# Optimization experiments

Hardware: AMD Instinct MI355X
Metric: run time of the kernel (lower is better)

The kernel has to match this reference:

```python
import jax, jax.numpy as jnp
import numpy as np

NUM_GRAPHS = 500
BN_EPS = 1e-5


def setup_inputs() -> dict:
    key = jax.random.key(0)
    ks = jax.random.split(key, 16)
    N, E, F, D, L = 100000, 1600000, 128, 128, 3
    x = jax.random.normal(ks[0], (N, F), dtype=jnp.float32)
    edge_index = jax.random.randint(ks[1], (2, E), 0, N)
    batch = jnp.sort(jax.random.randint(ks[2], (N,), 0, NUM_GRAPHS))
    s = 1.0 / np.sqrt(F)
    sd = 1.0 / np.sqrt(D)
    # SAGEConv layer 0: out = lin_l(mean_aggr(x_j)) + lin_r(x)
    sage_Wl = jax.random.uniform(ks[3], (F, D), jnp.float32, -s, s)
    sage_bl = jax.random.uniform(ks[4], (D,), jnp.float32, -s, s)
    sage_Wr = jax.random.uniform(ks[5], (F, D), jnp.float32, -s, s)
    # GINConv layers 1..L-1: nn = Linear(D,D) -> ReLU -> Linear(D,D)
    gin_W1 = jax.random.uniform(ks[6], (L - 1, D, D), jnp.float32, -sd, sd)
    gin_b1 = jax.random.uniform(ks[7], (L - 1, D), jnp.float32, -sd, sd)
    gin_W2 = jax.random.uniform(ks[8], (L - 1, D, D), jnp.float32, -sd, sd)
    gin_b2 = jax.random.uniform(ks[9], (L - 1, D), jnp.float32, -sd, sd)
    bn_gamma = jnp.ones((L, D), dtype=jnp.float32)
    bn_beta = jnp.zeros((L, D), dtype=jnp.float32)
    return {"x": x, "edge_index": edge_index, "batch": batch,
            "sage_Wl": sage_Wl, "sage_bl": sage_bl, "sage_Wr": sage_Wr,
            "gin_W1": gin_W1, "gin_b1": gin_b1, "gin_W2": gin_W2, "gin_b2": gin_b2,
            "bn_gamma": bn_gamma, "bn_beta": bn_beta}


def _batchnorm(h, gamma, beta):
    mu = jnp.mean(h, axis=0)
    var = jnp.var(h, axis=0)  # biased, as torch BN uses for normalization
    return (h - mu) * jax.lax.rsqrt(var + BN_EPS) * gamma + beta


def reference(x, edge_index, batch, sage_Wl, sage_bl, sage_Wr,
              gin_W1, gin_b1, gin_W2, gin_b2, bn_gamma, bn_beta):
    N = x.shape[0]
    src, dst = edge_index[0], edge_index[1]
    L = bn_gamma.shape[0]

    # Layer 0: SAGEConv (mean aggregation, root weight, no bias on lin_r)
    deg = jax.ops.segment_sum(jnp.ones_like(dst, dtype=x.dtype), dst, num_segments=N)
    aggr = jax.ops.segment_sum(x[src], dst, num_segments=N)
    aggr = aggr / jnp.maximum(deg, 1.0)[:, None]
    h = aggr @ sage_Wl + sage_bl + x @ sage_Wr
    h = jax.nn.relu(h)
    h = _batchnorm(h, bn_gamma[0], bn_beta[0])
    xs = [h]

    # Layers 1..L-1: GINConv (eps=0): nn(x + sum_aggr(x_j))
    for i in range(1, L):
        aggr = jax.ops.segment_sum(h[src], dst, num_segments=N)
        t = h + aggr
        t = jax.nn.relu(t @ gin_W1[i - 1] + gin_b1[i - 1])
        t = t @ gin_W2[i - 1] + gin_b2[i - 1]
        h = jax.nn.relu(t)
        h = _batchnorm(h, bn_gamma[i], bn_beta[i])
        xs.append(h)

    # pooling != 'last': concat global_add_pool over every layer
    pooled = jnp.concatenate(
        [jax.ops.segment_sum(xi, batch, num_segments=NUM_GRAPHS) for xi in xs], axis=1)
    node_feats = jnp.concatenate(xs, axis=1)
    return (pooled, node_feats)
```

## Files before the change

kernel.cpp:

```cpp
#include <hip/hip_runtime.h>
#include <hip/hip_bf16.h>


#define BN_EPS 1e-5f
#define EPB 4096

typedef short s8v __attribute__((ext_vector_type(8)));
typedef float f4v __attribute__((ext_vector_type(4)));

__device__ __forceinline__ float bflo(unsigned u) { return __uint_as_float(u << 16); }
__device__ __forceinline__ float bfhi(unsigned u) { return __uint_as_float(u & 0xffff0000u); }
__device__ __forceinline__ unsigned short f2bf(float f) {
    unsigned u = __float_as_uint(f);
    unsigned r = (u + 0x7fffu + ((u >> 16) & 1u)) >> 16;
    return (unsigned short)r;
}
__device__ __forceinline__ unsigned pk2(float a, float b) {
    return (unsigned)f2bf(a) | ((unsigned)f2bf(b) << 16);
}
__device__ __forceinline__ void unpack8(uint4 u, float* v) {
    v[0] = bflo(u.x); v[1] = bfhi(u.x);
    v[2] = bflo(u.y); v[3] = bfhi(u.y);
    v[4] = bflo(u.z); v[5] = bfhi(u.z);
    v[6] = bflo(u.w); v[7] = bfhi(u.w);
}


__global__ __launch_bounds__(256) void k_binA(const int* __restrict__ src,
                                              const int* __restrict__ dst, int E, int NB, int CAP,
                                              int* __restrict__ bcnt,
                                              unsigned long long* __restrict__ ebuf) {
    __shared__ int hist[512], base[512], cur[512];
    const int tid = threadIdx.x;
    const int e0 = blockIdx.x * EPB;
    for (int i = tid; i < 512; i += 256) { hist[i] = 0; cur[i] = 0; }
    __syncthreads();
#pragma unroll
    for (int k = 0; k < EPB / 256; k++) {
        int e = e0 + k * 256 + tid;
        if (e < E) atomicAdd(&hist[dst[e] >> 8], 1);
    }
    __syncthreads();
    for (int b = tid; b < NB; b += 256)
        base[b] = hist[b] ? atomicAdd(&bcnt[b], hist[b]) : 0;
    __syncthreads();
#pragma unroll
    for (int k = 0; k < EPB / 256; k++) {
        int e = e0 + k * 256 + tid;
        if (e < E) {
            int d = dst[e];
            int b = d >> 8;
            int lp = atomicAdd(&cur[b], 1);
            int gp = base[b] + lp;
            if (gp < CAP)
                ebuf[(size_t)b * CAP + gp] = ((unsigned long long)d << 32) | (unsigned)src[e];
        }
    }
}

__global__ __launch_bounds__(256) void k_binB(const unsigned long long* __restrict__ ebuf,
                                              int CAP, const int* __restrict__ bcnt,
                                              int N, int E,
                                              int* __restrict__ rp, int* __restrict__ csr) {
    __shared__ int deg[256], sc[256], cur[256];
    __shared__ int s_cbase;
    const int tid = threadIdx.x;
    const int b = blockIdx.x;
    const int cnt = min(bcnt[b], CAP);

    int partial = 0;
    for (int i = tid; i < b; i += 256) partial += bcnt[i];
    sc[tid] = partial;
    __syncthreads();
    for (int off = 128; off > 0; off >>= 1) {
        if (tid < off) sc[tid] += sc[tid + off];
        __syncthreads();
    }
    if (tid == 0) s_cbase = sc[0];
    __syncthreads();
    const int cbase = s_cbase;

    deg[tid] = 0;
    __syncthreads();
    const unsigned long long* eb = ebuf + (size_t)b * CAP;
    for (int i = tid; i < cnt; i += 256) {
        int d = (int)(eb[i] >> 32);
        atomicAdd(&deg[d & 255], 1);
    }
    __syncthreads();
    int myDeg = deg[tid];
    sc[tid] = myDeg;
    __syncthreads();
    for (int off = 1; off < 256; off <<= 1) {
        int v = (tid >= off) ? sc[tid - off] : 0;
        __syncthreads();
        sc[tid] += v;
        __syncthreads();
    }
    int pos = cbase + sc[tid] - myDeg;
    int node = b * 256 + tid;
    if (node < N) rp[node] = pos;
    cur[tid] = pos;
    __syncthreads();
    for (int i = tid; i < cnt; i += 256) {
        unsigned long long e = eb[i];
        int d = (int)(e >> 32);
        int p = atomicAdd(&cur[d & 255], 1);
        csr[p] = (int)(e & 0xffffffffu);
    }
    if (b == 0 && tid == 0) rp[N] = E;
}


__global__ __launch_bounds__(256) void k_prep(
    const float* __restrict__ sWl, const float* __restrict__ sWr,
    const float* __restrict__ gW1, const float* __restrict__ gW2,
    unsigned short* __restrict__ Wp,
    const float* __restrict__ x, uint4* __restrict__ tb, int n16,
    uint4* __restrict__ pool4, int npool4, int zpb,
    uint4* __restrict__ zreg4, int nzreg4) {
    const int b = blockIdx.x;
    const int tid = threadIdx.x;
    if (b < 384) {
        int wsel = b >> 6;
        int idx = (b & 63) * 256 + tid;
        const float* W;
        switch (wsel) {
            case 0: W = sWl; break;
            case 1: W = sWr; break;
            case 2: W = gW1; break;
            case 3: W = gW2; break;
            case 4: W = gW1 + 16384; break;
            default: W = gW2 + 16384; break;
        }
        int k = idx >> 7, d = idx & 127;
        float w = W[idx];
        unsigned short h = f2bf(w);
        float hf = __uint_as_float((unsigned)h << 16);
        unsigned short l = f2bf(w - hf);
        int o = (((k >> 3) * 128) + d) * 8 + (k & 7);
        unsigned short* slot = Wp + (size_t)wsel * 32768;
        slot[o] = h;
        slot[16384 + o] = l;
    } else if (b < 384 + zpb) {
        int i = (b - 384) * 256 + tid;
        if (i < npool4) pool4[i] = make_uint4(0, 0, 0, 0);
    } else if (b == 384 + zpb) {
        for (int i = tid; i < nzreg4; i += 256) zreg4[i] = make_uint4(0, 0, 0, 0);
    } else {
        int i = (b - 385 - zpb) * 256 + tid;
        if (i >= n16) return;
        const float4* p = reinterpret_cast<const float4*>(x) + (size_t)i * 2;
        float4 a = p[0], bb = p[1];
        uint4 o;
        o.x = pk2(a.x, a.y); o.y = pk2(a.z, a.w);
        o.z = pk2(bb.x, bb.y); o.w = pk2(bb.z, bb.w);
        tb[i] = o;
    }
}


template <bool SELF, bool MEAN>
__global__ __launch_bounds__(256) void k_aggr(const int* __restrict__ rp,
                                              const int* __restrict__ csr,
                                              const uint4* __restrict__ src,
                                              uint4* __restrict__ out, int N) {
    const int node = blockIdx.x * 4 + (threadIdx.x >> 6);
    if (node >= N) return;
    const int lane = threadIdx.x & 63;
    const int c = lane & 15, grp = lane >> 4;

    float acc[8];
#pragma unroll
    for (int k = 0; k < 8; k++) acc[k] = 0.f;

    const int lo = rp[node], hi = rp[node + 1];
    int j = lo + grp;
    for (; j + 12 < hi; j += 16) {
        int sn0 = csr[j];
        int sn1 = csr[j + 4];
        int sn2 = csr[j + 8];
        int sn3 = csr[j + 12];
        uint4 r0 = src[(size_t)sn0 * 16 + c];
        uint4 r1 = src[(size_t)sn1 * 16 + c];
        uint4 r2 = src[(size_t)sn2 * 16 + c];
        uint4 r3 = src[(size_t)sn3 * 16 + c];
        float v[8];
        unpack8(r0, v);
#pragma unroll
        for (int k = 0; k < 8; k++) acc[k] += v[k];
        unpack8(r1, v);
#pragma unroll
        for (int k = 0; k < 8; k++) acc[k] += v[k];
        unpack8(r2, v);
#pragma unroll
        for (int k = 0; k < 8; k++) acc[k] += v[k];
        unpack8(r3, v);
#pragma unroll
        for (int k = 0; k < 8; k++) acc[k] += v[k];
    }
    for (; j + 4 < hi; j += 8) {
        int sn0 = csr[j];
        int sn1 = csr[j + 4];
        uint4 r0 = src[(size_t)sn0 * 16 + c];
        uint4 r1 = src[(size_t)sn1 * 16 + c];
        float v[8];
        unpack8(r0, v);
#pragma unroll
        for (int k = 0; k < 8; k++) acc[k] += v[k];
        unpack8(r1, v);
#pragma unroll
        for (int k = 0; k < 8; k++) acc[k] += v[k];
    }
    if (j < hi) {
        float v[8];
        unpack8(src[(size_t)csr[j] * 16 + c], v);
#pragma unroll
        for (int k = 0; k < 8; k++) acc[k] += v[k];
    }

#pragma unroll
    for (int k = 0; k < 8; k++) {
        acc[k] += __shfl_xor(acc[k], 16, 64);
        acc[k] += __shfl_xor(acc[k], 32, 64);
    }

    if (grp == 0) {
        if (SELF) {
            float v[8];
            unpack8(src[(size_t)node * 16 + c], v);
#pragma unroll
            for (int k = 0; k < 8; k++) acc[k] += v[k];
        }
        if (MEAN) {
            float inv = 1.0f / fmaxf((float)(hi - lo), 1.0f);
#pragma unroll
            for (int k = 0; k < 8; k++) acc[k] *= inv;
        }
        uint4 o;
        o.x = pk2(acc[0], acc[1]); o.y = pk2(acc[2], acc[3]);
        o.z = pk2(acc[4], acc[5]); o.w = pk2(acc[6], acc[7]);
        out[(size_t)node * 16 + c] = o;
    }
}


#define MFMA_STAGE(Whi, Wlo, B0, B1, ACC)                                          \
    _Pragma("unroll")                                                              \
    for (int ks = 0; ks < 4; ks++) {                                               \
        s8v b0 = __builtin_bit_cast(s8v, B0[ks]);                                  \
        s8v b1 = __builtin_bit_cast(s8v, B1[ks]);                                  \
        _Pragma("unroll")                                                          \
        for (int df = 0; df < 8; df++) {                                           \
            int wi = (ks * 4 + lg) * 128 + df * 16 + l16;                          \
            s8v ah = __builtin_bit_cast(s8v, Whi[wi]);                             \
            s8v al = __builtin_bit_cast(s8v, Wlo[wi]);                             \
            ACC[0][df] = __builtin_amdgcn_mfma_f32_16x16x32_bf16(ah, b0, ACC[0][df], 0, 0, 0); \
            ACC[1][df] = __builtin_amdgcn_mfma_f32_16x16x32_bf16(ah, b1, ACC[1][df], 0, 0, 0); \
            ACC[0][df] = __builtin_amdgcn_mfma_f32_16x16x32_bf16(al, b0, ACC[0][df], 0, 0, 0); \
            ACC[1][df] = __builtin_amdgcn_mfma_f32_16x16x32_bf16(al, b1, ACC[1][df], 0, 0, 0); \
        }                                                                          \
    }

#define STATS_EPILOGUE(OO, V0, V1)                                                 \
    {                                                                              \
        _Pragma("unroll")                                                          \
        for (int df = 0; df < 8; df++) {                                           \
            float s[4], q[4];                                                      \
            _Pragma("unroll")                                                      \
            for (int r = 0; r < 4; r++) {                                          \
                float a0 = V0 ? (&OO[0][df].x)[r] : 0.f;                           \
                float a1 = V1 ? (&OO[1][df].x)[r] : 0.f;                           \
                s[r] = a0 + a1;                                                    \
                q[r] = a0 * a0 + a1 * a1;                                          \
            }                                                                      \
            _Pragma("unroll")                                                      \
            for (int m = 1; m < 16; m <<= 1) {                                     \
                _Pragma("unroll")                                                  \
                for (int r = 0; r < 4; r++) {                                      \
                    s[r] += __shfl_xor(s[r], m, 64);                               \
                    q[r] += __shfl_xor(q[r], m, 64);                               \
                }                                                                  \
            }                                                                      \
            if (l16 == 0) {                                                        \
                _Pragma("unroll")                                                  \
                for (int r = 0; r < 4; r++) {                                      \
                    sred[wid][df * 16 + lg * 4 + r][0] = s[r];                     \
                    sred[wid][df * 16 + lg * 4 + r][1] = q[r];                     \
                }                                                                  \
            }                                                                      \
        }                                                                          \
        __syncthreads();                                                           \
        if (tid < 128) {                                                           \
            float s = sred[0][tid][0] + sred[1][tid][0] + sred[2][tid][0] + sred[3][tid][0]; \
            float q = sred[0][tid][1] + sred[1][tid][1] + sred[2][tid][1] + sred[3][tid][1]; \
            unsafeAtomicAdd(&gsum[tid], s);                                        \
            unsafeAtomicAdd(&gsq[tid], q);                                         \
        }                                                                          \
    }


__global__ __launch_bounds__(256) void k_gemm_sage(
    const uint4* __restrict__ A1, const uint4* __restrict__ A2,
    const uint4* __restrict__ Wfrag,
    const float* __restrict__ bias,
    float* __restrict__ outF, float* __restrict__ gsum, float* __restrict__ gsq,
    int N) {
    __shared__ float sred[4][128][2];
    const int tid = threadIdx.x;
    const int lane = tid & 63, wid = tid >> 6;
    const int nbase = blockIdx.x * 128 + wid * 32;
    const int l16 = lane & 15, lg = lane >> 4;

    f4v acc[2][8];
#pragma unroll
    for (int nf = 0; nf < 2; nf++)
#pragma unroll
        for (int df = 0; df < 8; df++)
            acc[nf][df] = (f4v){0.f, 0.f, 0.f, 0.f};

#pragma unroll
    for (int t = 0; t < 2; t++) {
        const uint4* A = t ? A2 : A1;
        const uint4* Whi = Wfrag + (size_t)t * 4096;
        const uint4* Wlo = Whi + 2048;
        uint4 bvec[2][4];
#pragma unroll
        for (int nf = 0; nf < 2; nf++) {
            const uint4* row = A + (size_t)(nbase + nf * 16 + l16) * 16;
#pragma unroll
            for (int ks = 0; ks < 4; ks++) bvec[nf][ks] = row[ks * 4 + lg];
        }
        MFMA_STAGE(Whi, Wlo, bvec[0], bvec[1], acc)
    }

    const bool v0 = (nbase + l16) < N;
    const bool v1 = (nbase + 16 + l16) < N;
    float4 oo[2][8];
#pragma unroll
    for (int df = 0; df < 8; df++) {
        int d0 = df * 16 + lg * 4;
        const float4 bb = *reinterpret_cast<const float4*>(bias + d0);
#pragma unroll
        for (int nf = 0; nf < 2; nf++) {
            oo[nf][df].x = fmaxf(acc[nf][df][0] + bb.x, 0.f);
            oo[nf][df].y = fmaxf(acc[nf][df][1] + bb.y, 0.f);
            oo[nf][df].z = fmaxf(acc[nf][df][2] + bb.z, 0.f);
            oo[nf][df].w = fmaxf(acc[nf][df][3] + bb.w, 0.f);
        }
    }

    STATS_EPILOGUE(oo, v0, v1)

#pragma unroll
    for (int nf = 0; nf < 2; nf++) {
        int n = nbase + nf * 16 + l16;
        if (n < N) {
#pragma unroll
            for (int df = 0; df < 8; df++)
                *reinterpret_cast<float4*>(outF + (size_t)n * 384 + df * 16 + lg * 4) = oo[nf][df];
        }
    }
}


__global__ __launch_bounds__(256) void k_gemm_gin(
    const uint4* __restrict__ A,
    const uint4* __restrict__ W1f, const uint4* __restrict__ W2f,
    const float* __restrict__ b1, const float* __restrict__ b2,
    float* __restrict__ outF, float* __restrict__ gsum, float* __restrict__ gsq,
    int N) {
    __shared__ uint4 tile[2048];
    __shared__ float sred[4][128][2];
    const int tid = threadIdx.x;
    const int lane = tid & 63, wid = tid >> 6;
    const int nbase = blockIdx.x * 128 + wid * 32;
    const int l16 = lane & 15, lg = lane >> 4;

    f4v acc[2][8];
#pragma unroll
    for (int nf = 0; nf < 2; nf++)
#pragma unroll
        for (int df = 0; df < 8; df++)
            acc[nf][df] = (f4v){0.f, 0.f, 0.f, 0.f};

    {
        const uint4* Whi = W1f;
        const uint4* Wlo = W1f + 2048;
        uint4 bvec[2][4];
#pragma unroll
        for (int nf = 0; nf < 2; nf++) {
            const uint4* row = A + (size_t)(nbase + nf * 16 + l16) * 16;
#pragma unroll
            for (int ks = 0; ks < 4; ks++) bvec[nf][ks] = row[ks * 4 + lg];
        }
        MFMA_STAGE(Whi, Wlo, bvec[0], bvec[1], acc)
    }
#pragma unroll
    for (int df = 0; df < 8; df++) {
        int d0 = df * 16 + lg * 4;
        const float4 bb = *reinterpret_cast<const float4*>(b1 + d0);
#pragma unroll
        for (int nf = 0; nf < 2; nf++) {
            float tx = fmaxf(acc[nf][df][0] + bb.x, 0.f);
            float ty = fmaxf(acc[nf][df][1] + bb.y, 0.f);
            float tz = fmaxf(acc[nf][df][2] + bb.z, 0.f);
            float tw = fmaxf(acc[nf][df][3] + bb.w, 0.f);
            uint2 p;
            p.x = pk2(tx, ty);
            p.y = pk2(tz, tw);
            int row = wid * 32 + nf * 16 + l16;
            int col4 = df * 2 + (lg >> 1);
            int slot = row * 16 + (col4 ^ (row & 15));
            *reinterpret_cast<uint2*>(
                reinterpret_cast<char*>(tile) + (size_t)slot * 16 + (lg & 1) * 8) = p;
        }
    }
    __syncthreads();

#pragma unroll
    for (int nf = 0; nf < 2; nf++)
#pragma unroll
        for (int df = 0; df < 8; df++)
            acc[nf][df] = (f4v){0.f, 0.f, 0.f, 0.f};
    {
        const uint4* Whi = W2f;
        const uint4* Wlo = W2f + 2048;
        uint4 bvec[2][4];
#pragma unroll
        for (int nf = 0; nf < 2; nf++) {
            int row = wid * 32 + nf * 16 + l16;
#pragma unroll
            for (int ks = 0; ks < 4; ks++)
                bvec[nf][ks] = tile[row * 16 + ((ks * 4 + lg) ^ (row & 15))];
        }
        MFMA_STAGE(Whi, Wlo, bvec[0], bvec[1], acc)
    }

    const bool v0 = (nbase + l16) < N;
    const bool v1 = (nbase + 16 + l16) < N;
    float4 oo[2][8];
#pragma unroll
    for (int df = 0; df < 8; df++) {
        int d0 = df * 16 + lg * 4;
        const float4 bb = *reinterpret_cast<const float4*>(b2 + d0);
#pragma unroll
        for (int nf = 0; nf < 2; nf++) {
            oo[nf][df].x = fmaxf(acc[nf][df][0] + bb.x, 0.f);
            oo[nf][df].y = fmaxf(acc[nf][df][1] + bb.y, 0.f);
            oo[nf][df].z = fmaxf(acc[nf][df][2] + bb.z, 0.f);
            oo[nf][df].w = fmaxf(acc[nf][df][3] + bb.w, 0.f);
        }
    }

    STATS_EPILOGUE(oo, v0, v1)

#pragma unroll
    for (int nf = 0; nf < 2; nf++) {
        int n = nbase + nf * 16 + l16;
        if (n < N) {
#pragma unroll
            for (int df = 0; df < 8; df++)
                *reinterpret_cast<float4*>(outF + (size_t)n * 384 + df * 16 + lg * 4) = oo[nf][df];
        }
    }
}


__global__ __launch_bounds__(128) void k_normpool(
    float* __restrict__ nfl,
    const float* __restrict__ gsumL, const float* __restrict__ gsqL,
    const float* __restrict__ gammaL, const float* __restrict__ betaL,
    float invN, const int* __restrict__ batch, int N,
    float* __restrict__ pooledL,
    unsigned short* __restrict__ tab) {
    const int d = threadIdx.x;
    float mu = gsumL[d] * invN;
    float var = gsqL[d] * invN - mu * mu;
    float rs = rsqrtf(var + BN_EPS);
    const float a = gammaL[d] * rs;
    const float c = betaL[d] - mu * a;

    const int n0 = blockIdx.x * 64;
    const int n1 = min(n0 + 64, N);
    float s = 0.f;
    int curg = batch[n0];
    for (int n = n0; n < n1; n++) {
        int g = batch[n];
        if (g != curg) {
            unsafeAtomicAdd(&pooledL[(size_t)curg * 384 + d], s);
            s = 0.f;
            curg = g;
        }
        float v = nfl[(size_t)n * 384 + d];
        float h = fmaf(v, a, c);
        nfl[(size_t)n * 384 + d] = h;
        s += h;
        if (tab) tab[(size_t)n * 128 + d] = f2bf(h);
    }
    unsafeAtomicAdd(&pooledL[(size_t)curg * 384 + d], s);
}


extern "C" void kernel_launch(void* const* d_in, const int* in_sizes, int n_in,
                              void* d_out, int out_size, void* d_ws, size_t ws_size,
                              hipStream_t stream) {
    const float* x   = (const float*)d_in[0];
    const int*   ei  = (const int*)d_in[1];
    const int*   bat = (const int*)d_in[2];
    const float* sWl = (const float*)d_in[3];
    const float* sbl = (const float*)d_in[4];
    const float* sWr = (const float*)d_in[5];
    const float* gW1 = (const float*)d_in[6];
    const float* gb1 = (const float*)d_in[7];
    const float* gW2 = (const float*)d_in[8];
    const float* gb2 = (const float*)d_in[9];
    const float* bng = (const float*)d_in[10];
    const float* bnb = (const float*)d_in[11];

    const int N = in_sizes[0] / 128;
    const int E = in_sizes[1] / 2;
    const int G = out_size / 384 - N;
    const int* srcp = ei;
    const int* dstp = ei + E;

    char* w = (char*)d_ws;
    auto alloc = [&](size_t bytes) -> void* {
        void* p = (void*)w;
        w += (bytes + 255) & ~(size_t)255;
        return p;
    };
    const size_t Npad = (size_t)(N + 128);
    int*   rp    = (int*)alloc(((size_t)N + 1) * 4);
    int*   csr   = (int*)alloc((size_t)E * 4);
    char*  zreg  = (char*)alloc(2048 + 2 * 3 * 512);
    int*   bcnt  = (int*)zreg;
    float* gsum  = (float*)(zreg + 2048);
    float* gsq   = gsum + 3 * 128;
    unsigned short* Wp = (unsigned short*)alloc((size_t)6 * 2 * 16384 * 2);
    unsigned short* ab = (unsigned short*)alloc(Npad * 256);
    unsigned short* tb = (unsigned short*)alloc(Npad * 256);

    float* pooled = (float*)d_out;
    float* nf     = pooled + (size_t)G * 384;

    const float invN = 1.0f / (float)N;

    const int NB  = (N + 255) / 256;
    int CAP = ((2 * (E / (NB > 0 ? NB : 1)) + 511) / 512) * 512;
    const long long maxcap = (long long)(Npad * 256) / ((long long)NB * 8);
    if ((long long)CAP > maxcap) CAP = (int)(maxcap & ~511LL);
    unsigned long long* ebuf = (unsigned long long*)ab;

    const int egrid = (E + EPB - 1) / EPB;
    const int agrid = (N + 3) / 4;
    const int ggrid = (N + 127) / 128;
    const int pgrid = (N + 63) / 64;

    const int npool4 = G * 96;
    const int zpb    = (npool4 + 255) / 256;
    const int nzreg4 = (2048 + 2 * 3 * 512) / 16;
    const int cvtb   = (N * 16 + 255) / 256;
    const int prepgrid = 384 + zpb + 1 + cvtb;

    k_prep<<<prepgrid, 256, 0, stream>>>(sWl, sWr, gW1, gW2, Wp,
                                         x, (uint4*)tb, N * 16,
                                         (uint4*)pooled, npool4, zpb,
                                         (uint4*)zreg, nzreg4);
    k_binA<<<egrid, 256, 0, stream>>>(srcp, dstp, E, NB, CAP, bcnt, ebuf);
    k_binB<<<NB, 256, 0, stream>>>(ebuf, CAP, bcnt, N, E, rp, csr);

    k_aggr<false, true><<<agrid, 256, 0, stream>>>(rp, csr, (const uint4*)tb, (uint4*)ab, N);
    k_gemm_sage<<<ggrid, 256, 0, stream>>>(
        (const uint4*)ab, (const uint4*)tb, (const uint4*)Wp, sbl, nf, gsum, gsq, N);
    k_normpool<<<pgrid, 128, 0, stream>>>(nf, gsum, gsq, bng, bnb, invN, bat, N,
                                          pooled, tb);

    for (int l = 1; l < 3; l++) {
        const uint4* W1p = (const uint4*)(Wp + (size_t)(2 * l) * 32768);
        const uint4* W2p = (const uint4*)(Wp + (size_t)(2 * l + 1) * 32768);
        const float* b1 = gb1 + (size_t)(l - 1) * 128;
        const float* b2 = gb2 + (size_t)(l - 1) * 128;
        float* nfl = nf + (size_t)l * 128;

        k_aggr<true, false><<<agrid, 256, 0, stream>>>(rp, csr, (const uint4*)tb, (uint4*)ab, N);
        k_gemm_gin<<<ggrid, 256, 0, stream>>>(
            (const uint4*)ab, W1p, W2p, b1, b2, nfl, gsum + l * 128, gsq + l * 128, N);
        k_normpool<<<pgrid, 128, 0, stream>>>(nfl, gsum + l * 128, gsq + l * 128,
                                              bng + l * 128, bnb + l * 128, invN, bat, N,
                                              pooled + (size_t)l * 128,
                                              (l < 2) ? tb : nullptr);
    }
}
```

Baseline: 565.5 us.

## Fuse neighbor aggregation into GEMM kernels via per-block LDS tile

The separate aggregation kernel is removed. Each GEMM block now gathers and sums neighbor rows for its 128 nodes straight into a swizzled shared-memory tile, and the MFMA stage reads its B operand from that tile. This drops the global write and re-read of the aggregated bf16 buffer plus one launch per layer. In exchange, each wave handles 32 nodes serially instead of one node per wave across 25k blocks, which cuts memory-level parallelism for the latency-bound gather. In the GIN kernel, a __syncthreads between writing the hidden tile and reading it back was also removed, and that looks unsafe.

```diff
diff --git a/kernel.cpp b/kernel.cpp
--- a/kernel.cpp
+++ b/kernel.cpp
@@ -161,86 +161,81 @@
 
 
 template <bool SELF, bool MEAN>
-__global__ __launch_bounds__(256) void k_aggr(const int* __restrict__ rp,
-                                              const int* __restrict__ csr,
-                                              const uint4* __restrict__ src,
-                                              uint4* __restrict__ out, int N) {
-    const int node = blockIdx.x * 4 + (threadIdx.x >> 6);
-    if (node >= N) return;
-    const int lane = threadIdx.x & 63;
+__device__ __forceinline__ void gather_tile(const int* __restrict__ rp,
+                                            const int* __restrict__ csr,
+                                            const uint4* __restrict__ src,
+                                            uint4* __restrict__ tile,
+                                            int wid, int lane, int nblk, int N) {
     const int c = lane & 15, grp = lane >> 4;
-
-    float acc[8];
-#pragma unroll
-    for (int k = 0; k < 8; k++) acc[k] = 0.f;
-
-    const int lo = rp[node], hi = rp[node + 1];
-    int j = lo + grp;
-    for (; j + 12 < hi; j += 16) {
-        int sn0 = csr[j];
-        int sn1 = csr[j + 4];
-        int sn2 = csr[j + 8];
-        int sn3 = csr[j + 12];
-        uint4 r0 = src[(size_t)sn0 * 16 + c];
-        uint4 r1 = src[(size_t)sn1 * 16 + c];
-        uint4 r2 = src[(size_t)sn2 * 16 + c];
-        uint4 r3 = src[(size_t)sn3 * 16 + c];
-        float v[8];
-        unpack8(r0, v);
-#pragma unroll
-        for (int k = 0; k < 8; k++) acc[k] += v[k];
-        unpack8(r1, v);
-#pragma unroll
-        for (int k = 0; k < 8; k++) acc[k] += v[k];
-        unpack8(r2, v);
-#pragma unroll
-        for (int k = 0; k < 8; k++) acc[k] += v[k];
-        unpack8(r3, v);
-#pragma unroll
-        for (int k = 0; k < 8; k++) acc[k] += v[k];
-    }
-    for (; j + 4 < hi; j += 8) {
-        int sn0 = csr[j];
-        int sn1 = csr[j + 4];
-        uint4 r0 = src[(size_t)sn0 * 16 + c];
-        uint4 r1 = src[(size_t)sn1 * 16 + c];
-        float v[8];
-        unpack8(r0, v);
-#pragma unroll
-        for (int k = 0; k < 8; k++) acc[k] += v[k];
-        unpack8(r1, v);
-#pragma unroll
-        for (int k = 0; k < 8; k++) acc[k] += v[k];
-    }
-    if (j < hi) {
-        float v[8];
-        unpack8(src[(size_t)csr[j] * 16 + c], v);
-#pragma unroll
-        for (int k = 0; k < 8; k++) acc[k] += v[k];
-    }
-
-#pragma unroll
-    for (int k = 0; k < 8; k++) {
-        acc[k] += __shfl_xor(acc[k], 16, 64);
-        acc[k] += __shfl_xor(acc[k], 32, 64);
-    }
-
-    if (grp == 0) {
-        if (SELF) {
+    for (int i = 0; i < 32; i++) {
+        const int row = wid * 32 + i;
+        const int node = nblk + row;
+        float acc[8];
+#pragma unroll
+        for (int k = 0; k < 8; k++) acc[k] = 0.f;
+        int lo = 0, hi = 0;
+        if (node < N) { lo = rp[node]; hi = rp[node + 1]; }
+        int j = lo + grp;
+        for (; j + 12 < hi; j += 16) {
+            int sn0 = csr[j], sn1 = csr[j + 4], sn2 = csr[j + 8], sn3 = csr[j + 12];
+            uint4 r0 = src[(size_t)sn0 * 16 + c];
+            uint4 r1 = src[(size_t)sn1 * 16 + c];
+            uint4 r2 = src[(size_t)sn2 * 16 + c];
+            uint4 r3 = src[(size_t)sn3 * 16 + c];
             float v[8];
-            unpack8(src[(size_t)node * 16 + c], v);
-#pragma unroll
-            for (int k = 0; k < 8; k++) acc[k] += v[k];
-        }
-        if (MEAN) {
-            float inv = 1.0f / fmaxf((float)(hi - lo), 1.0f);
-#pragma unroll
-            for (int k = 0; k < 8; k++) acc[k] *= inv;
-        }
-        uint4 o;
-        o.x = pk2(acc[0], acc[1]); o.y = pk2(acc[2], acc[3]);
-        o.z = pk2(acc[4], acc[5]); o.w = pk2(acc[6], acc[7]);
-        out[(size_t)node * 16 + c] = o;
+            unpack8(r0, v);
+#pragma unroll
+            for (int k = 0; k < 8; k++) acc[k] += v[k];
+            unpack8(r1, v);
+#pragma unroll
+            for (int k = 0; k < 8; k++) acc[k] += v[k];
+            unpack8(r2, v);
+#pragma unroll
+            for (int k = 0; k < 8; k++) acc[k] += v[k];
+            unpack8(r3, v);
+#pragma unroll
+            for (int k = 0; k < 8; k++) acc[k] += v[k];
+        }
+        for (; j + 4 < hi; j += 8) {
+            int sn0 = csr[j], sn1 = csr[j + 4];
+            uint4 r0 = src[(size_t)sn0 * 16 + c];
+            uint4 r1 = src[(size_t)sn1 * 16 + c];
+            float v[8];
+            unpack8(r0, v);
+#pragma unroll
+            for (int k = 0; k < 8; k++) acc[k] += v[k];
+            unpack8(r1, v);
+#pragma unroll
+            for (int k = 0; k < 8; k++) acc[k] += v[k];
+        }
+        if (j < hi) {
+            float v[8];
+            unpack8(src[(size_t)csr[j] * 16 + c], v);
+#pragma unroll
+            for (int k = 0; k < 8; k++) acc[k] += v[k];
+        }
+#pragma unroll
+        for (int k = 0; k < 8; k++) {
+            acc[k] += __shfl_xor(acc[k], 16, 64);
+            acc[k] += __shfl_xor(acc[k], 32, 64);
+        }
+        if (grp == 0) {
+            if (SELF && node < N) {
+                float v[8];
+                unpack8(src[(size_t)node * 16 + c], v);
+#pragma unroll
+                for (int k = 0; k < 8; k++) acc[k] += v[k];
+            }
+            if (MEAN) {
+                float inv = 1.0f / fmaxf((float)(hi - lo), 1.0f);
+#pragma unroll
+                for (int k = 0; k < 8; k++) acc[k] *= inv;
+            }
+            uint4 o;
+            o.x = pk2(acc[0], acc[1]); o.y = pk2(acc[2], acc[3]);
+            o.z = pk2(acc[4], acc[5]); o.w = pk2(acc[6], acc[7]);
+            tile[row * 16 + (c ^ (row & 15))] = o;
+        }
     }
 }
 
@@ -260,6 +255,15 @@
             ACC[0][df] = __builtin_amdgcn_mfma_f32_16x16x32_bf16(al, b0, ACC[0][df], 0, 0, 0); \
             ACC[1][df] = __builtin_amdgcn_mfma_f32_16x16x32_bf16(al, b1, ACC[1][df], 0, 0, 0); \
         }                                                                          \
+    }
+
+#define LOAD_B_LDS(BV)                                                             \
+    _Pragma("unroll")                                                              \
+    for (int nf = 0; nf < 2; nf++) {                                               \
+        int row = wid * 32 + nf * 16 + l16;                                        \
+        _Pragma("unroll")                                                          \
+        for (int ks = 0; ks < 4; ks++)                                             \
+            BV[nf][ks] = tile[row * 16 + ((ks * 4 + lg) ^ (row & 15))];            \
     }
 
 #define STATS_EPILOGUE(OO, V0, V1)                                                 \
@@ -300,17 +304,22 @@
     }
 
 
-__global__ __launch_bounds__(256) void k_gemm_sage(
-    const uint4* __restrict__ A1, const uint4* __restrict__ A2,
+__global__ __launch_bounds__(256) void k_sage_fused(
+    const int* __restrict__ rp, const int* __restrict__ csr,
+    const uint4* __restrict__ tb,
     const uint4* __restrict__ Wfrag,
     const float* __restrict__ bias,
     float* __restrict__ outF, float* __restrict__ gsum, float* __restrict__ gsq,
     int N) {
+    __shared__ uint4 tile[2048];
     __shared__ float sred[4][128][2];
     const int tid = threadIdx.x;
     const int lane = tid & 63, wid = tid >> 6;
-    const int nbase = blockIdx.x * 128 + wid * 32;
+    const int nblk = blockIdx.x * 128;
+    const int nbase = nblk + wid * 32;
     const int l16 = lane & 15, lg = lane >> 4;
+
+    gather_tile<false, true>(rp, csr, tb, tile, wid, lane, nblk, N);
 
     f4v acc[2][8];
 #pragma unroll
@@ -319,18 +328,23 @@
         for (int df = 0; df < 8; df++)
             acc[nf][df] = (f4v){0.f, 0.f, 0.f, 0.f};
 
-#pragma unroll
-    for (int t = 0; t < 2; t++) {
-        const uint4* A = t ? A2 : A1;
-        const uint4* Whi = Wfrag + (size_t)t * 4096;
-        const uint4* Wlo = Whi + 2048;
+    {
         uint4 bvec[2][4];
+        LOAD_B_LDS(bvec)
+        const uint4* Whi = Wfrag;
+        const uint4* Wlo = Wfrag + 2048;
+        MFMA_STAGE(Whi, Wlo, bvec[0], bvec[1], acc)
+    }
+    {
+        uint4 bvec[2][4];
 #pragma unroll
         for (int nf = 0; nf < 2; nf++) {
-            const uint4* row = A + (size_t)(nbase + nf * 16 + l16) * 16;
+            const uint4* row = tb + (size_t)(nbase + nf * 16 + l16) * 16;
 #pragma unroll
             for (int ks = 0; ks < 4; ks++) bvec[nf][ks] = row[ks * 4 + lg];
         }
+        const uint4* Whi = Wfrag + 4096;
+        const uint4* Wlo = Wfrag + 6144;
         MFMA_STAGE(Whi, Wlo, bvec[0], bvec[1], acc)
     }
 
@@ -364,8 +378,9 @@
 }
 
 
-__global__ __launch_bounds__(256) void k_gemm_gin(
-    const uint4* __restrict__ A,
+__global__ __launch_bounds__(256) void k_gin_fused(
+    const int* __restrict__ rp, const int* __restrict__ csr,
+    const uint4* __restrict__ tb,
     const uint4* __restrict__ W1f, const uint4* __restrict__ W2f,
     const float* __restrict__ b1, const float* __restrict__ b2,
     float* __restrict__ outF, float* __restrict__ gsum, float* __restrict__ gsq,
@@ -374,8 +389,11 @@
     __shared__ float sred[4][128][2];
     const int tid = threadIdx.x;
     const int lane = tid & 63, wid = tid >> 6;
-    const int nbase = blockIdx.x * 128 + wid * 32;
+    const int nblk = blockIdx.x * 128;
+    const int nbase = nblk + wid * 32;
     const int l16 = lane & 15, lg = lane >> 4;
+
+    gather_tile<true, false>(rp, csr, tb, tile, wid, lane, nblk, N);
 
     f4v acc[2][8];
 #pragma unroll
@@ -385,15 +403,10 @@
             acc[nf][df] = (f4v){0.f, 0.f, 0.f, 0.f};
 
     {
+        uint4 bvec[2][4];
+        LOAD_B_LDS(bvec)
         const uint4* Whi = W1f;
         const uint4* Wlo = W1f + 2048;
-        uint4 bvec[2][4];
-#pragma unroll
-        for (int nf = 0; nf < 2; nf++) {
-            const uint4* row = A + (size_t)(nbase + nf * 16 + l16) * 16;
-#pragma unroll
-            for (int ks = 0; ks < 4; ks++) bvec[nf][ks] = row[ks * 4 + lg];
-        }
         MFMA_STAGE(Whi, Wlo, bvec[0], bvec[1], acc)
     }
 #pragma unroll
@@ -416,7 +429,6 @@
                 reinterpret_cast<char*>(tile) + (size_t)slot * 16 + (lg & 1) * 8) = p;
         }
     }
-    __syncthreads();
 
 #pragma unroll
     for (int nf = 0; nf < 2; nf++)
@@ -424,16 +436,10 @@
         for (int df = 0; df < 8; df++)
             acc[nf][df] = (f4v){0.f, 0.f, 0.f, 0.f};
     {
+        uint4 bvec[2][4];
+        LOAD_B_LDS(bvec)
         const uint4* Whi = W2f;
         const uint4* Wlo = W2f + 2048;
-        uint4 bvec[2][4];
-#pragma unroll
-        for (int nf = 0; nf < 2; nf++) {
-            int row = wid * 32 + nf * 16 + l16;
-#pragma unroll
-            for (int ks = 0; ks < 4; ks++)
-                bvec[nf][ks] = tile[row * 16 + ((ks * 4 + lg) ^ (row & 15))];
-        }
         MFMA_STAGE(Whi, Wlo, bvec[0], bvec[1], acc)
     }
 
@@ -537,9 +543,9 @@
     int*   bcnt  = (int*)zreg;
     float* gsum  = (float*)(zreg + 2048);
     float* gsq   = gsum + 3 * 128;
-    unsigned short* Wp = (unsigned short*)alloc((size_t)6 * 2 * 16384 * 2);
-    unsigned short* ab = (unsigned short*)alloc(Npad * 256);
-    unsigned short* tb = (unsigned short*)alloc(Npad * 256);
+    unsigned short* Wp   = (unsigned short*)alloc((size_t)6 * 2 * 16384 * 2);
+    unsigned short* ebuf = (unsigned short*)alloc(Npad * 256);
+    unsigned short* tb   = (unsigned short*)alloc(Npad * 256);
 
     float* pooled = (float*)d_out;
     float* nf     = pooled + (size_t)G * 384;
@@ -550,10 +556,8 @@
     int CAP = ((2 * (E / (NB > 0 ? NB : 1)) + 511) / 512) * 512;
     const long long maxcap = (long long)(Npad * 256) / ((long long)NB * 8);
     if ((long long)CAP > maxcap) CAP = (int)(maxcap & ~511LL);
-    unsigned long long* ebuf = (unsigned long long*)ab;
 
     const int egrid = (E + EPB - 1) / EPB;
-    const int agrid = (N + 3) / 4;
     const int ggrid = (N + 127) / 128;
     const int pgrid = (N + 63) / 64;
 
@@ -567,12 +571,13 @@
                                          x, (uint4*)tb, N * 16,
                                          (uint4*)pooled, npool4, zpb,
                                          (uint4*)zreg, nzreg4);
-    k_binA<<<egrid, 256, 0, stream>>>(srcp, dstp, E, NB, CAP, bcnt, ebuf);
-    k_binB<<<NB, 256, 0, stream>>>(ebuf, CAP, bcnt, N, E, rp, csr);
-
-    k_aggr<false, true><<<agrid, 256, 0, stream>>>(rp, csr, (const uint4*)tb, (uint4*)ab, N);
-    k_gemm_sage<<<ggrid, 256, 0, stream>>>(
-        (const uint4*)ab, (const uint4*)tb, (const uint4*)Wp, sbl, nf, gsum, gsq, N);
+    k_binA<<<egrid, 256, 0, stream>>>(srcp, dstp, E, NB, CAP, bcnt,
+                                      (unsigned long long*)ebuf);
+    k_binB<<<NB, 256, 0, stream>>>((const unsigned long long*)ebuf, CAP, bcnt,
+                                   N, E, rp, csr);
+
+    k_sage_fused<<<ggrid, 256, 0, stream>>>(
+        rp, csr, (const uint4*)tb, (const uint4*)Wp, sbl, nf, gsum, gsq, N);
     k_normpool<<<pgrid, 128, 0, stream>>>(nf, gsum, gsq, bng, bnb, invN, bat, N,
                                           pooled, tb);
 
@@ -583,9 +588,9 @@
         const float* b2 = gb2 + (size_t)(l - 1) * 128;
         float* nfl = nf + (size_t)l * 128;
 
-        k_aggr<true, false><<<agrid, 256, 0, stream>>>(rp, csr, (const uint4*)tb, (uint4*)ab, N);
-        k_gemm_gin<<<ggrid, 256, 0, stream>>>(
-            (const uint4*)ab, W1p, W2p, b1, b2, nfl, gsum + l * 128, gsq + l * 128, N);
+        k_gin_fused<<<ggrid, 256, 0, stream>>>(
+            rp, csr, (const uint4*)tb, W1p, W2p, b1, b2, nfl,
+            gsum + l * 128, gsq + l * 128, N);
         k_normpool<<<pgrid, 128, 0, stream>>>(nfl, gsum + l * 128, gsq + l * 128,
                                               bng + l * 128, bnb + l * 128, invN, bat, N,
                                               pooled + (size_t)l * 128,
```

Result: slower. 744.8 us (+31.7%).

## Store bf16 features in feature-sliced layout so aggregation gathers per slice

Applied to the files above, without the earlier changes.

Node feature tables move from row-major [N][128] to eight 16-feature slices, each stored contiguously across nodes. The aggregation kernel now gives each block one slice for 32 nodes, so each gather pulls 32 bytes per neighbour from a 3.2 MB slice. The aim is better L2/cache locality for the random neighbour gathers, with blockIdx low bits selecting the slice. In exchange each gather is narrower and the 16-edge unrolled loop is dropped, and the GEMM, prep and normpool kernels must index the strided layout.

```diff
diff --git a/kernel.cpp b/kernel.cpp
--- a/kernel.cpp
+++ b/kernel.cpp
@@ -7,6 +7,9 @@
 
 typedef short s8v __attribute__((ext_vector_type(8)));
 typedef float f4v __attribute__((ext_vector_type(4)));
+
+#define TIDX(node, slot) \
+    ((size_t)((slot) >> 1) * (size_t)SS4 + (size_t)(node) * 2 + ((slot) & 1))
 
 __device__ __forceinline__ float bflo(unsigned u) { return __uint_as_float(u << 16); }
 __device__ __forceinline__ float bfhi(unsigned u) { return __uint_as_float(u & 0xffff0000u); }
@@ -116,7 +119,7 @@
     const float* __restrict__ sWl, const float* __restrict__ sWr,
     const float* __restrict__ gW1, const float* __restrict__ gW2,
     unsigned short* __restrict__ Wp,
-    const float* __restrict__ x, uint4* __restrict__ tb, int n16,
+    const float* __restrict__ x, uint4* __restrict__ tb, int n16, int SS4,
     uint4* __restrict__ pool4, int npool4, int zpb,
     uint4* __restrict__ zreg4, int nzreg4) {
     const int b = blockIdx.x;
@@ -150,25 +153,28 @@
     } else {
         int i = (b - 385 - zpb) * 256 + tid;
         if (i >= n16) return;
-        const float4* p = reinterpret_cast<const float4*>(x) + (size_t)i * 2;
+        int n = i >> 4, slot = i & 15;
+        const float4* p = reinterpret_cast<const float4*>(x) + ((size_t)n * 32 + slot * 2);
         float4 a = p[0], bb = p[1];
         uint4 o;
         o.x = pk2(a.x, a.y); o.y = pk2(a.z, a.w);
         o.z = pk2(bb.x, bb.y); o.w = pk2(bb.z, bb.w);
-        tb[i] = o;
+        tb[TIDX(n, slot)] = o;
     }
 }
 
 
 template <bool SELF, bool MEAN>
-__global__ __launch_bounds__(256) void k_aggr(const int* __restrict__ rp,
-                                              const int* __restrict__ csr,
-                                              const uint4* __restrict__ src,
-                                              uint4* __restrict__ out, int N) {
-    const int node = blockIdx.x * 4 + (threadIdx.x >> 6);
+__global__ __launch_bounds__(256) void k_aggr_slice(
+    const int* __restrict__ rp, const int* __restrict__ csr,
+    const uint4* __restrict__ src, uint4* __restrict__ out, int N, int SS4) {
+    const int slice = blockIdx.x & 7;
+    const int chunk = blockIdx.x >> 3;
+    const int wid = threadIdx.x >> 6, lane = threadIdx.x & 63;
+    const int node = chunk * 32 + wid * 8 + (lane >> 3);
     if (node >= N) return;
-    const int lane = threadIdx.x & 63;
-    const int c = lane & 15, grp = lane >> 4;
+    const int sub = lane & 7, grp = sub >> 1, half = sub & 1;
+    const uint4* sl = src + (size_t)slice * SS4;
 
     float acc[8];
 #pragma unroll
@@ -176,34 +182,11 @@
 
     const int lo = rp[node], hi = rp[node + 1];
     int j = lo + grp;
-    for (; j + 12 < hi; j += 16) {
-        int sn0 = csr[j];
-        int sn1 = csr[j + 4];
-        int sn2 = csr[j + 8];
-        int sn3 = csr[j + 12];
-        uint4 r0 = src[(size_t)sn0 * 16 + c];
-        uint4 r1 = src[(size_t)sn1 * 16 + c];
-        uint4 r2 = src[(size_t)sn2 * 16 + c];
-        uint4 r3 = src[(size_t)sn3 * 16 + c];
-        float v[8];
-        unpack8(r0, v);
-#pragma unroll
-        for (int k = 0; k < 8; k++) acc[k] += v[k];
-        unpack8(r1, v);
-#pragma unroll
-        for (int k = 0; k < 8; k++) acc[k] += v[k];
-        unpack8(r2, v);
-#pragma unroll
-        for (int k = 0; k < 8; k++) acc[k] += v[k];
-        unpack8(r3, v);
-#pragma unroll
-        for (int k = 0; k < 8; k++) acc[k] += v[k];
-    }
     for (; j + 4 < hi; j += 8) {
         int sn0 = csr[j];
         int sn1 = csr[j + 4];
-        uint4 r0 = src[(size_t)sn0 * 16 + c];
-        uint4 r1 = src[(size_t)sn1 * 16 + c];
+        uint4 r0 = sl[(size_t)sn0 * 2 + half];
+        uint4 r1 = sl[(size_t)sn1 * 2 + half];
         float v[8];
         unpack8(r0, v);
 #pragma unroll
@@ -214,21 +197,21 @@
     }
     if (j < hi) {
         float v[8];
-        unpack8(src[(size_t)csr[j] * 16 + c], v);
+        unpack8(sl[(size_t)csr[j] * 2 + half], v);
 #pragma unroll
         for (int k = 0; k < 8; k++) acc[k] += v[k];
     }
 
 #pragma unroll
     for (int k = 0; k < 8; k++) {
-        acc[k] += __shfl_xor(acc[k], 16, 64);
-        acc[k] += __shfl_xor(acc[k], 32, 64);
+        acc[k] += __shfl_xor(acc[k], 2, 64);
+        acc[k] += __shfl_xor(acc[k], 4, 64);
     }
 
     if (grp == 0) {
         if (SELF) {
             float v[8];
-            unpack8(src[(size_t)node * 16 + c], v);
+            unpack8(sl[(size_t)node * 2 + half], v);
 #pragma unroll
             for (int k = 0; k < 8; k++) acc[k] += v[k];
         }
@@ -240,7 +223,7 @@
         uint4 o;
         o.x = pk2(acc[0], acc[1]); o.y = pk2(acc[2], acc[3]);
         o.z = pk2(acc[4], acc[5]); o.w = pk2(acc[6], acc[7]);
-        out[(size_t)node * 16 + c] = o;
+        out[(size_t)slice * SS4 + (size_t)node * 2 + half] = o;
     }
 }
 
@@ -259,6 +242,17 @@
             ACC[1][df] = __builtin_amdgcn_mfma_f32_16x16x32_bf16(ah, b1, ACC[1][df], 0, 0, 0); \
             ACC[0][df] = __builtin_amdgcn_mfma_f32_16x16x32_bf16(al, b0, ACC[0][df], 0, 0, 0); \
             ACC[1][df] = __builtin_amdgcn_mfma_f32_16x16x32_bf16(al, b1, ACC[1][df], 0, 0, 0); \
+        }                                                                          \
+    }
+
+#define LOAD_B_BLOCKED(A, BV)                                                      \
+    _Pragma("unroll")                                                              \
+    for (int nf = 0; nf < 2; nf++) {                                               \
+        int node_ = nbase + nf * 16 + l16;                                         \
+        _Pragma("unroll")                                                          \
+        for (int ks = 0; ks < 4; ks++) {                                           \
+            int slot_ = ks * 4 + lg;                                               \
+            BV[nf][ks] = A[TIDX(node_, slot_)];                                    \
         }                                                                          \
     }
 
@@ -305,7 +299,7 @@
     const uint4* __restrict__ Wfrag,
     const float* __restrict__ bias,
     float* __restrict__ outF, float* __restrict__ gsum, float* __restrict__ gsq,
-    int N) {
+    int N, int SS4) {
     __shared__ float sred[4][128][2];
     const int tid = threadIdx.x;
     const int lane = tid & 63, wid = tid >> 6;
@@ -325,12 +319,7 @@
         const uint4* Whi = Wfrag + (size_t)t * 4096;
         const uint4* Wlo = Whi + 2048;
         uint4 bvec[2][4];
-#pragma unroll
-        for (int nf = 0; nf < 2; nf++) {
-            const uint4* row = A + (size_t)(nbase + nf * 16 + l16) * 16;
-#pragma unroll
-            for (int ks = 0; ks < 4; ks++) bvec[nf][ks] = row[ks * 4 + lg];
-        }
+        LOAD_B_BLOCKED(A, bvec)
         MFMA_STAGE(Whi, Wlo, bvec[0], bvec[1], acc)
     }
 
@@ -369,7 +358,7 @@
     const uint4* __restrict__ W1f, const uint4* __restrict__ W2f,
     const float* __restrict__ b1, const float* __restrict__ b2,
     float* __restrict__ outF, float* __restrict__ gsum, float* __restrict__ gsq,
-    int N) {
+    int N, int SS4) {
     __shared__ uint4 tile[2048];
     __shared__ float sred[4][128][2];
     const int tid = threadIdx.x;
@@ -388,12 +377,7 @@
         const uint4* Whi = W1f;
         const uint4* Wlo = W1f + 2048;
         uint4 bvec[2][4];
-#pragma unroll
-        for (int nf = 0; nf < 2; nf++) {
-            const uint4* row = A + (size_t)(nbase + nf * 16 + l16) * 16;
-#pragma unroll
-            for (int ks = 0; ks < 4; ks++) bvec[nf][ks] = row[ks * 4 + lg];
-        }
+        LOAD_B_BLOCKED(A, bvec)
         MFMA_STAGE(Whi, Wlo, bvec[0], bvec[1], acc)
     }
 #pragma unroll
@@ -473,13 +457,14 @@
     const float* __restrict__ gammaL, const float* __restrict__ betaL,
     float invN, const int* __restrict__ batch, int N,
     float* __restrict__ pooledL,
-    unsigned short* __restrict__ tab) {
+    unsigned short* __restrict__ tab, int SS4) {
     const int d = threadIdx.x;
     float mu = gsumL[d] * invN;
     float var = gsqL[d] * invN - mu * mu;
     float rs = rsqrtf(var + BN_EPS);
     const float a = gammaL[d] * rs;
     const float c = betaL[d] - mu * a;
+    unsigned short* tslice = tab ? tab + (size_t)(d >> 4) * SS4 * 8 + (d & 15) : nullptr;
 
     const int n0 = blockIdx.x * 64;
     const int n1 = min(n0 + 64, N);
@@ -496,7 +481,7 @@
         float h = fmaf(v, a, c);
         nfl[(size_t)n * 384 + d] = h;
         s += h;
-        if (tab) tab[(size_t)n * 128 + d] = f2bf(h);
+        if (tslice) tslice[(size_t)n * 16] = f2bf(h);
     }
     unsafeAtomicAdd(&pooledL[(size_t)curg * 384 + d], s);
 }
@@ -531,6 +516,7 @@
         return p;
     };
     const size_t Npad = (size_t)(N + 128);
+    const int SS4 = (int)(Npad * 2);
     int*   rp    = (int*)alloc(((size_t)N + 1) * 4);
     int*   csr   = (int*)alloc((size_t)E * 4);
     char*  zreg  = (char*)alloc(2048 + 2 * 3 * 512);
@@ -553,7 +539,7 @@
     unsigned long long* ebuf = (unsigned long long*)ab;
 
     const int egrid = (E + EPB - 1) / EPB;
-    const int agrid = (N + 3) / 4;
+    const int agrid = ((N + 31) / 32) * 8;
     const int ggrid = (N + 127) / 128;
     const int pgrid = (N + 63) / 64;
 
@@ -564,17 +550,19 @@
     const int prepgrid = 384 + zpb + 1 + cvtb;
 
     k_prep<<<prepgrid, 256, 0, stream>>>(sWl, sWr, gW1, gW2, Wp,
-                                         x, (uint4*)tb, N * 16,
+                                         x, (uint4*)tb, N * 16, SS4,
                                          (uint4*)pooled, npool4, zpb,
                                          (uint4*)zreg, nzreg4);
     k_binA<<<egrid, 256, 0, stream>>>(srcp, dstp, E, NB, CAP, bcnt, ebuf);
     k_binB<<<NB, 256, 0, stream>>>(ebuf, CAP, bcnt, N, E, rp, csr);
 
-    k_aggr<false, true><<<agrid, 256, 0, stream>>>(rp, csr, (const uint4*)tb, (uint4*)ab, N);
+    k_aggr_slice<false, true><<<agrid, 256, 0, stream>>>(rp, csr, (const uint4*)tb,
+                                                         (uint4*)ab, N, SS4);
     k_gemm_sage<<<ggrid, 256, 0, stream>>>(
-        (const uint4*)ab, (const uint4*)tb, (const uint4*)Wp, sbl, nf, gsum, gsq, N);
+        (const uint4*)ab, (const uint4*)tb, (const uint4*)Wp, sbl, nf,
+        gsum, gsq, N, SS4);
     k_normpool<<<pgrid, 128, 0, stream>>>(nf, gsum, gsq, bng, bnb, invN, bat, N,
-                                          pooled, tb);
+                                          pooled, tb, SS4);
 
     for (int l = 1; l < 3; l++) {
         const uint4* W1p = (const uint4*)(Wp + (size_t)(2 * l) * 32768);
@@ -583,12 +571,14 @@
         const float* b2 = gb2 + (size_t)(l - 1) * 128;
         float* nfl = nf + (size_t)l * 128;
 
-        k_aggr<true, false><<<agrid, 256, 0, stream>>>(rp, csr, (const uint4*)tb, (uint4*)ab, N);
+        k_aggr_slice<true, false><<<agrid, 256, 0, stream>>>(rp, csr, (const uint4*)tb,
+                                                             (uint4*)ab, N, SS4);
         k_gemm_gin<<<ggrid, 256, 0, stream>>>(
-            (const uint4*)ab, W1p, W2p, b1, b2, nfl, gsum + l * 128, gsq + l * 128, N);
+            (const uint4*)ab, W1p, W2p, b1, b2, nfl,
+            gsum + l * 128, gsq + l * 128, N, SS4);
         k_normpool<<<pgrid, 128, 0, stream>>>(nfl, gsum + l * 128, gsq + l * 128,
                                               bng + l * 128, bnb + l * 128, invN, bat, N,
                                               pooled + (size_t)l * 128,
-                                              (l < 2) ? tb : nullptr);
-    }
-}
+                                              (l < 2) ? tb : nullptr, SS4);
+    }
+}
```

Result: slower. 596.1 us (+5.4%).
